# Kernel optimization log

Measured on AMD Instinct MI355X. Metric: run time of the kernel, lower is better.

The kernel has to match this reference:

```python
import jax, jax.numpy as jnp
import numpy as np

B = 1024          # batch size (rows, and diagonal positives)
Q = 65536         # gps queue length
K = B + Q         # total logits columns


def setup_inputs() -> dict:
    key = jax.random.key(0)
    logits = jax.random.normal(key, (B, K), dtype=jnp.float32)
    return {"logits": logits, "batch_size": B}


def reference(logits, batch_size):
    # logits: [B, K], K = batch_size + queue_len. Diagonal [i, i] = positive pair.
    Bsz = batch_size
    Kcols = logits.shape[1]
    rows = jnp.arange(Bsz)
    diag_mask = jnp.eye(Bsz, Kcols, dtype=bool)          # True on positives

    # hard-negative weights: exp(detached logits), mean taken over off-diagonal only
    hw = jnp.exp(jax.lax.stop_gradient(logits))          # [B, K]
    diag_hw = hw[rows, rows]                             # [B]
    neg_mean = (hw.sum(axis=-1) - diag_hw) / (Kcols - 1) # mean over K-1 negatives
    norm_w = hw / neg_mean[:, None]                      # [B, K]

    # replace off-diagonal logits with weighted versions, keep diagonal as-is
    updated = jnp.where(diag_mask, logits, logits * norm_w)

    # CrossEntropyLoss with targets = arange(B), mean reduction
    logp = jax.nn.log_softmax(updated, axis=-1)          # [B, K]
    loss = -jnp.mean(logp[rows, rows])
    return loss
```

## Files before the change

### kernel.cpp

```cpp
#include <hip/hip_runtime.h>
#include <math.h>


#define TPB 512
#define NWAVES (TPB / 64)

__global__ __launch_bounds__(TPB) void wl_row_kernel(const float* __restrict__ logits,
                                                     float* __restrict__ row_loss,
                                                     int B, int K) {
    __shared__ float sh_s[NWAVES];
    __shared__ float sh_g[NWAVES];
    __shared__ float sh_bc[3];

    const int tid  = threadIdx.x;
    const int lane = tid & 63;
    const int wid  = tid >> 6;
    const int K4   = K >> 2;

    for (int r = blockIdx.x; r < B; r += gridDim.x) {
        const float4* __restrict__ row4 = (const float4*)(logits + (size_t)r * (size_t)K);

        float s = 0.0f;
        float g = -INFINITY;
        for (int i = tid; i < K4; i += TPB) {
            float4 v = row4[i];
            float e0 = __expf(v.x), e1 = __expf(v.y), e2 = __expf(v.z), e3 = __expf(v.w);
            s += (e0 + e1) + (e2 + e3);
            g = fmaxf(g, fmaxf(fmaxf(v.x * e0, v.y * e1), fmaxf(v.z * e2, v.w * e3)));
        }
        #pragma unroll
        for (int off = 32; off > 0; off >>= 1) {
            s += __shfl_down(s, off);
            g = fmaxf(g, __shfl_down(g, off));
        }
        if (lane == 0) { sh_s[wid] = s; sh_g[wid] = g; }
        __syncthreads();
        if (tid == 0) {
            float st = 0.0f, gt = -INFINITY;
            #pragma unroll
            for (int w = 0; w < NWAVES; ++w) { st += sh_s[w]; gt = fmaxf(gt, sh_g[w]); }
            float d  = logits[(size_t)r * (size_t)K + (size_t)r];
            float ed = __expf(d);
            float neg_mean = (st - ed) / (float)(K - 1);
            float c = 1.0f / neg_mean;
            float M = fmaxf(d, c * gt);
            sh_bc[0] = c; sh_bc[1] = M; sh_bc[2] = d;
        }
        __syncthreads();
        const float c = sh_bc[0];
        const float M = sh_bc[1];
        const float d = sh_bc[2];

        float z = 0.0f;
        for (int i = tid; i < K4; i += TPB) {
            float4 v = row4[i];
            const int col = i << 2;
            float e0 = __expf(v.x), e1 = __expf(v.y), e2 = __expf(v.z), e3 = __expf(v.w);
            float u0 = fmaf(c, v.x * e0, -M);
            float u1 = fmaf(c, v.y * e1, -M);
            float u2 = fmaf(c, v.z * e2, -M);
            float u3 = fmaf(c, v.w * e3, -M);
            if (col     == r) u0 = d - M;
            if (col + 1 == r) u1 = d - M;
            if (col + 2 == r) u2 = d - M;
            if (col + 3 == r) u3 = d - M;
            z += (__expf(u0) + __expf(u1)) + (__expf(u2) + __expf(u3));
        }
        #pragma unroll
        for (int off = 32; off > 0; off >>= 1) z += __shfl_down(z, off);
        if (lane == 0) sh_s[wid] = z;
        __syncthreads();
        if (tid == 0) {
            float zt = 0.0f;
            #pragma unroll
            for (int w = 0; w < NWAVES; ++w) zt += sh_s[w];
            row_loss[r] = M + logf(zt) - d;
        }
        __syncthreads();
    }
}

__global__ __launch_bounds__(256) void wl_final_kernel(const float* __restrict__ row_loss,
                                                       float* __restrict__ out, int B) {
    __shared__ float sh[4];
    const int tid = threadIdx.x;
    float s = 0.0f;
    for (int i = tid; i < B; i += 256) s += row_loss[i];
    #pragma unroll
    for (int off = 32; off > 0; off >>= 1) s += __shfl_down(s, off);
    const int lane = tid & 63, wid = tid >> 6;
    if (lane == 0) sh[wid] = s;
    __syncthreads();
    if (tid == 0) {
        out[0] = (sh[0] + sh[1] + sh[2] + sh[3]) / (float)B;
    }
}

extern "C" void kernel_launch(void* const* d_in, const int* in_sizes, int n_in,
                              void* d_out, int out_size, void* d_ws, size_t ws_size,
                              hipStream_t stream) {
    const float* logits = (const float*)d_in[0];
    const int B = 1024;
    const int K = in_sizes[0] / B;
    float* ws  = (float*)d_ws;
    float* out = (float*)d_out;

    wl_row_kernel<<<512, TPB, 0, stream>>>(logits, ws, B, K);
    wl_final_kernel<<<1, 256, 0, stream>>>(ws, out, B);
}
```

Measured before the change: 399.4 us.

## Cache per-row weighted logits in LDS as fp16, refetch only significant entries

During the first pass each row's x*exp(x) values are packed into an fp16 shared-memory buffer sized for the whole row. The second pass reads that buffer instead of re-reading the row from global memory. It recomputes in fp32 from global only the entries whose shifted value exceeds -34, which are the only ones that contribute meaningfully to the softmax sum. The block size doubles to 1024 threads and the grid becomes one block per row; the roughly 130KB of LDS per block limits occupancy to one block per CU, and the code assumes K is at most KMAX.

```diff
diff --git a/kernel.cpp b/kernel.cpp
--- a/kernel.cpp
+++ b/kernel.cpp
@@ -1,13 +1,16 @@
 #include <hip/hip_runtime.h>
+#include <hip/hip_fp16.h>
 #include <math.h>
 
 
-#define TPB 512
+#define TPB 1024
 #define NWAVES (TPB / 64)
+#define KMAX 66560
 
-__global__ __launch_bounds__(TPB) void wl_row_kernel(const float* __restrict__ logits,
-                                                     float* __restrict__ row_loss,
-                                                     int B, int K) {
+__global__ __launch_bounds__(TPB, 1) void wl_row_kernel(const float* __restrict__ logits,
+                                                        float* __restrict__ row_loss,
+                                                        int B, int K) {
+    __shared__ __align__(16) __half g16[KMAX];
     __shared__ float sh_s[NWAVES];
     __shared__ float sh_g[NWAVES];
     __shared__ float sh_bc[3];
@@ -18,15 +21,21 @@
     const int K4   = K >> 2;
 
     for (int r = blockIdx.x; r < B; r += gridDim.x) {
-        const float4* __restrict__ row4 = (const float4*)(logits + (size_t)r * (size_t)K);
+        const float* __restrict__ row  = logits + (size_t)r * (size_t)K;
+        const float4* __restrict__ row4 = (const float4*)row;
 
         float s = 0.0f;
         float g = -INFINITY;
         for (int i = tid; i < K4; i += TPB) {
             float4 v = row4[i];
             float e0 = __expf(v.x), e1 = __expf(v.y), e2 = __expf(v.z), e3 = __expf(v.w);
+            float g0 = v.x * e0, g1 = v.y * e1, g2 = v.z * e2, g3 = v.w * e3;
             s += (e0 + e1) + (e2 + e3);
-            g = fmaxf(g, fmaxf(fmaxf(v.x * e0, v.y * e1), fmaxf(v.z * e2, v.w * e3)));
+            g = fmaxf(g, fmaxf(fmaxf(g0, g1), fmaxf(g2, g3)));
+            union { __half2 h[2]; float2 f; } pk;
+            pk.h[0] = __floats2half2_rn(g0, g1);
+            pk.h[1] = __floats2half2_rn(g2, g3);
+            ((float2*)g16)[i] = pk.f;
         }
         #pragma unroll
         for (int off = 32; off > 0; off >>= 1) {
@@ -39,7 +48,7 @@
             float st = 0.0f, gt = -INFINITY;
             #pragma unroll
             for (int w = 0; w < NWAVES; ++w) { st += sh_s[w]; gt = fmaxf(gt, sh_g[w]); }
-            float d  = logits[(size_t)r * (size_t)K + (size_t)r];
+            float d  = row[r];
             float ed = __expf(d);
             float neg_mean = (st - ed) / (float)(K - 1);
             float c = 1.0f / neg_mean;
@@ -53,13 +62,19 @@
 
         float z = 0.0f;
         for (int i = tid; i < K4; i += TPB) {
-            float4 v = row4[i];
+            union { __half2 h[2]; float2 f; } pk;
+            pk.f = ((const float2*)g16)[i];
+            float2 g01 = __half22float2(pk.h[0]);
+            float2 g23 = __half22float2(pk.h[1]);
+            float u0 = fmaf(c, g01.x, -M);
+            float u1 = fmaf(c, g01.y, -M);
+            float u2 = fmaf(c, g23.x, -M);
+            float u3 = fmaf(c, g23.y, -M);
             const int col = i << 2;
-            float e0 = __expf(v.x), e1 = __expf(v.y), e2 = __expf(v.z), e3 = __expf(v.w);
-            float u0 = fmaf(c, v.x * e0, -M);
-            float u1 = fmaf(c, v.y * e1, -M);
-            float u2 = fmaf(c, v.z * e2, -M);
-            float u3 = fmaf(c, v.w * e3, -M);
+            if (u0 > -34.0f) { float lf = row[col    ]; u0 = fmaf(c, lf * __expf(lf), -M); }
+            if (u1 > -34.0f) { float lf = row[col + 1]; u1 = fmaf(c, lf * __expf(lf), -M); }
+            if (u2 > -34.0f) { float lf = row[col + 2]; u2 = fmaf(c, lf * __expf(lf), -M); }
+            if (u3 > -34.0f) { float lf = row[col + 3]; u3 = fmaf(c, lf * __expf(lf), -M); }
             if (col     == r) u0 = d - M;
             if (col + 1 == r) u1 = d - M;
             if (col + 2 == r) u2 = d - M;
@@ -105,6 +120,6 @@
     float* ws  = (float*)d_ws;
     float* out = (float*)d_out;
 
-    wl_row_kernel<<<512, TPB, 0, stream>>>(logits, ws, B, K);
+    wl_row_kernel<<<B, TPB, 0, stream>>>(logits, ws, B, K);
     wl_final_kernel<<<1, 256, 0, stream>>>(ws, out, B);
 }
```

After: 382.5 us. 4.2% less time.
